# Performance work log

Measured on AMD Instinct MI355X. Metric: run time of the kernel, lower is better.

The kernel has to match this reference:

```python
import jax, jax.numpy as jnp
import numpy as np

B, N, F, H, N_ITERS = 64, 256, 16, 256, 10


def setup_inputs() -> dict:
    key = jax.random.key(0)
    ks = jax.random.split(key, 20)
    s = 0.05
    jets = jax.random.normal(ks[0], (B, N, F), dtype=jnp.float32)
    # row-normalized dense adjacency (D^-1 A style)
    a = jax.random.uniform(ks[1], (B, N, N), dtype=jnp.float32)
    dads = a / jnp.sum(a, axis=-1, keepdims=True)
    p = lambda k, sh: jax.random.normal(k, sh, dtype=jnp.float32) * s
    return {
        'jets': jets, 'dads': dads,
        'W_emb': p(ks[2], (F, H)), 'b_emb': jnp.zeros((H,), jnp.float32),
        'W_msg': p(ks[3], (H, H)), 'b_msg': jnp.zeros((H,), jnp.float32),
        # GRU vertex update: input = concat(message[H], s[F]) -> H
        'Wz': p(ks[4], (H + F, H)), 'Uz': p(ks[5], (H, H)), 'bz': jnp.zeros((H,), jnp.float32),
        'Wr': p(ks[6], (H + F, H)), 'Ur': p(ks[7], (H, H)), 'br': jnp.zeros((H,), jnp.float32),
        'Wh': p(ks[8], (H + F, H)), 'Uh': p(ks[9], (H, H)), 'bh': jnp.zeros((H,), jnp.float32),
        'W_r1': p(ks[10], (H, H)), 'b_r1': jnp.zeros((H,), jnp.float32),
        'W_r2': p(ks[11], (H, H)), 'b_r2': jnp.zeros((H,), jnp.float32),
    }


def reference(jets, dads, W_emb, b_emb, W_msg, b_msg,
              Wz, Uz, bz, Wr, Ur, br, Wh, Uh, bh,
              W_r1, b_r1, W_r2, b_r2):
    # Embedding: [B,N,F] -> [B,N,H]
    h = jnp.tanh(jets @ W_emb + b_emb)
    for _ in range(N_ITERS):
        # Message: linear then adjacency aggregation + tanh
        m = jnp.tanh(jnp.matmul(dads, h @ W_msg + b_msg))  # [B,N,H]
        # GRU-style vertex update; input = concat(message, original features s)
        x = jnp.concatenate([m, jets], axis=-1)            # [B,N,H+F]
        z = jax.nn.sigmoid(x @ Wz + h @ Uz + bz)
        r = jax.nn.sigmoid(x @ Wr + h @ Ur + br)
        h_tilde = jnp.tanh(x @ Wh + (r * h) @ Uh + bh)
        h = (1.0 - z) * h + z * h_tilde
    # Readout: per-node MLP then sum over nodes -> [B,H]
    out = jnp.sum(jnp.tanh(h @ W_r1 + b_r1) @ W_r2 + b_r2, axis=1)
    return out
```

## Files before the change

kernel.cpp:

```cpp
#include <hip/hip_runtime.h>

#define DEVI __device__ __forceinline__

typedef __attribute__((ext_vector_type(4))) float f32x4;
typedef __attribute__((ext_vector_type(8))) short s16x8;
typedef __attribute__((ext_vector_type(4))) short s16x4;
typedef unsigned short u16;
typedef unsigned int u32;

#define WST 288
#define SROW 264
#define AST 260

#define WAITVM(n) __builtin_amdgcn_s_waitcnt(((n)&0xF) | 0x70 | 0xF00 | (((n)>>4)<<14))

DEVI u16 f2bf(float x){
  u32 u = __float_as_uint(x);
  u = (u + 0x7fffu + ((u >> 16) & 1u)) >> 16;
  return (u16)u;
}
DEVI float bf2f(u16 v){ return __uint_as_float(((u32)v) << 16); }

DEVI float fsigm(float x){ return __builtin_amdgcn_rcpf(1.f + __builtin_amdgcn_exp2f(-1.442695041f * x)); }
DEVI float ftanh(float x){ float e = __builtin_amdgcn_exp2f(2.885390082f * x); return 1.f - 2.f * __builtin_amdgcn_rcpf(e + 1.f); }

DEVI s16x8 ld8(const u16* p){ return *(const s16x8*)p; }
DEVI s16x8 ldb64p(const u16* p){
  s16x4 lo = *(const s16x4*)p;
  s16x4 hi = *(const s16x4*)(p + 4);
  s16x8 r;
  r[0]=lo[0]; r[1]=lo[1]; r[2]=lo[2]; r[3]=lo[3];
  r[4]=hi[0]; r[5]=hi[1]; r[6]=hi[2]; r[7]=hi[3];
  return r;
}

DEVI f32x4 ld4bf(const u16* p){
  uint2 v = *(const uint2*)p;
  f32x4 r;
  r[0] = bf2f((u16)(v.x & 0xffff)); r[1] = bf2f((u16)(v.x >> 16));
  r[2] = bf2f((u16)(v.y & 0xffff)); r[3] = bf2f((u16)(v.y >> 16));
  return r;
}

DEVI void st4bf(u16* p, float a, float b, float c, float d){
  uint2 v;
  v.x = (u32)f2bf(a) | ((u32)f2bf(b) << 16);
  v.y = (u32)f2bf(c) | ((u32)f2bf(d) << 16);
  *(uint2*)p = v;
}

#define MFMA(a,b,c) __builtin_amdgcn_mfma_f32_16x16x32_bf16((a),(b),(c),0,0,0)

DEVI void dma4(const u16* lanebase, int rowStrideElems, int c, u16* ldsbase){
#pragma unroll
  for(int q = 0; q < 4; q++){
    const u16* g = lanebase + (size_t)q*16*rowStrideElems + c*32;
    __builtin_amdgcn_global_load_lds((__attribute__((address_space(1))) const void*)g,
                                     (__attribute__((address_space(3))) void*)(ldsbase + q*512),
                                     16, 0, 0);
  }
}
#define AFRAG(buf, t) ld8(&(buf)[(t)*512 + ln*32 + ((qd ^ ((ln>>1)&3))*8)])

__global__ void k_prep(
  const float* __restrict__ jets, const float* __restrict__ dads, const float* __restrict__ W_emb,
  const float* __restrict__ W_msg, const float* __restrict__ Wz, const float* __restrict__ Uz,
  const float* __restrict__ Wr, const float* __restrict__ Ur, const float* __restrict__ Wh,
  const float* __restrict__ Uh, const float* __restrict__ W_r1,
  u16* __restrict__ jp, u16* __restrict__ dadsb, u16* __restrict__ Wet, u16* __restrict__ Wmt,
  u16* __restrict__ Wzt, u16* __restrict__ Uzt, u16* __restrict__ Wrt, u16* __restrict__ Urt,
  u16* __restrict__ Wht, u16* __restrict__ Uht, u16* __restrict__ Wr1t)
{
  int blk = blockIdx.x, tid = threadIdx.x;
  if(blk < 1280){
    int mi = blk >> 8, k = blk & 255, j = tid;
    const float* src; u16* dst;
    switch(mi){
      case 0: src = W_msg; dst = Wmt;  break;
      case 1: src = Uz;    dst = Uzt;  break;
      case 2: src = Ur;    dst = Urt;  break;
      case 3: src = Uh;    dst = Uht;  break;
      default: src = W_r1; dst = Wr1t; break;
    }
    dst[j*256 + k] = f2bf(src[k*256 + j]);
  } else if(blk < 2144){
    int q = blk - 1280; int mi = q / 288; int k = q - mi*288; int j = tid;
    const float* src; u16* dst;
    switch(mi){ case 0: src = Wz; dst = Wzt; break; case 1: src = Wr; dst = Wrt; break; default: src = Wh; dst = Wht; break; }
    dst[j*WST + k] = (k < 272) ? f2bf(src[k*256 + j]) : (u16)0;
  } else if(blk < 2176){
    int idx = (blk - 2144)*256 + tid;
    int j = idx >> 5, k = idx & 31;
    Wet[idx] = (k < 16) ? f2bf(W_emb[k*256 + j]) : (u16)0;
  } else if(blk < 4224){
    int idx = (blk - 2176)*256 + tid;
    int n = idx >> 5, k = idx & 31;
    jp[idx] = (k < 16) ? f2bf(jets[n*16 + k]) : (u16)0;
  } else {
    int idx = (blk - 4224)*256 + tid;
    f32x4 v = *(const f32x4*)(dads + (size_t)idx*4);
    st4bf(dadsb + (size_t)idx*4, v[0], v[1], v[2], v[3]);
  }
}

__global__ __launch_bounds__(256,3) void k_embed(
  u16* __restrict__ h, u16* __restrict__ hmo,
  const u16* __restrict__ jp, const u16* __restrict__ Wet, const float* __restrict__ be,
  const u16* __restrict__ Wmt, const float* __restrict__ bm)
{
  __shared__ u16 hbuf[16*SROW];
  const int tid = threadIdx.x;
  const int wv = tid >> 6, lane = tid & 63, ln = lane & 15, qd = lane >> 4;
  const int n0 = blockIdx.x * 16;
  const int b  = n0 >> 8;
  const int nb = n0 & 255;
  const int nodeA = n0 + ln;

  s16x8 jfr = ld8(jp + (size_t)nodeA*32 + qd*8);
#pragma unroll
  for(int t = 0; t < 4; t++){
    int j0 = (wv*4 + t) * 16;
    f32x4 acc = {0.f,0.f,0.f,0.f};
    s16x8 a = ld8(Wet + (size_t)(j0 + ln)*32 + qd*8);
    acc = MFMA(a, jfr, acc);
    f32x4 bv = *(const f32x4*)(be + j0 + qd*4);
    f32x4 hv;
#pragma unroll
    for(int r = 0; r < 4; r++) hv[r] = ftanh(acc[r] + bv[r]);
    st4bf(h + (size_t)nodeA*256 + j0 + qd*4, hv[0], hv[1], hv[2], hv[3]);
    st4bf(&hbuf[ln*SROW + j0 + qd*4], hv[0], hv[1], hv[2], hv[3]);
  }
  __syncthreads();

  s16x8 af[8];
#pragma unroll
  for(int c = 0; c < 8; c++) af[c] = ld8(&hbuf[ln*SROW + c*32 + qd*8]);
#pragma unroll
  for(int tp = 0; tp < 2; tp++){
    int j0 = (wv*4 + tp*2) * 16, j1 = j0 + 16;
    f32x4 a0 = {0.f,0.f,0.f,0.f}, a1 = {0.f,0.f,0.f,0.f};
#pragma unroll
    for(int c = 0; c < 8; c++){
      a0 = MFMA(af[c], ld8(Wmt + (size_t)(j0 + ln)*256 + c*32 + qd*8), a0);
      a1 = MFMA(af[c], ld8(Wmt + (size_t)(j1 + ln)*256 + c*32 + qd*8), a1);
    }
    float b0 = bm[j0 + ln], b1 = bm[j1 + ln];
    st4bf(hmo + (size_t)(b*256 + j0 + ln)*256 + nb + qd*4, a0[0]+b0, a0[1]+b0, a0[2]+b0, a0[3]+b0);
    st4bf(hmo + (size_t)(b*256 + j1 + ln)*256 + nb + qd*4, a1[0]+b1, a1[1]+b1, a1[2]+b1, a1[3]+b1);
  }
}

__global__ __launch_bounds__(256,1) void k_gru(
  u16* __restrict__ h,
  const u16* __restrict__ hmi, u16* __restrict__ hmo,
  const u16* __restrict__ dadsb, const u16* __restrict__ jp,
  const u16* __restrict__ Wzt, const u16* __restrict__ Wrt, const u16* __restrict__ Wht,
  const u16* __restrict__ Uzt, const u16* __restrict__ Urt, const u16* __restrict__ Uht,
  const u16* __restrict__ Wmt,
  const float* __restrict__ bz, const float* __restrict__ br, const float* __restrict__ bhb,
  const float* __restrict__ bm)
{
  __shared__ u16 smM[64*AST];
  __shared__ u16 smB[64*AST];
  __shared__ __align__(16) u16 stg[4][2][2][2048];
  const int tid = threadIdx.x;
  const int wv = tid >> 6, lane = tid & 63, ln = lane & 15, qd = lane >> 4;
  const int blk   = blockIdx.x;
  const int batch = (blk & 7) * 8 + (blk >> 5);
  const int group = (blk >> 3) & 3;
  const int n0 = batch * 256 + group * 64;
  const int b  = batch;
  const int nb = group * 64;
  const int j0w = wv * 64;

  u16* s0 = &stg[wv][0][0][0];
  u16* s1 = &stg[wv][1][0][0];
  u16* u0 = &stg[wv][0][1][0];
  u16* u1 = &stg[wv][1][1][0];

  const int rw = lane >> 2;
  const int cs = ((lane & 3) ^ ((lane >> 3) & 3)) * 8;

  const u16* laneA = hmi + (size_t)(b*256 + j0w + rw)*256 + cs;
  dma4(laneA, 256, 0, s0);

  s16x8 jB[4];
#pragma unroll
  for(int i = 0; i < 4; i++) jB[i] = ld8(jp + (size_t)(n0 + i*16 + ln)*32 + qd*8);

  {
    f32x4 acc[4][4];
#pragma unroll
    for(int t = 0; t < 4; t++)
#pragma unroll
      for(int i = 0; i < 4; i++) acc[t][i] = (f32x4){0.f,0.f,0.f,0.f};
    s16x8 Bf[4], Bn[4];
#pragma unroll
    for(int i = 0; i < 4; i++) Bf[i] = ld8(dadsb + (size_t)(n0 + i*16 + ln)*256 + qd*8);
#pragma unroll
    for(int c = 0; c < 8; c++){
      u16* cur = (c & 1) ? s1 : s0;
      if(c < 7){
        dma4(laneA, 256, c+1, (c & 1) ? s0 : s1);
#pragma unroll
        for(int i = 0; i < 4; i++) Bn[i] = ld8(dadsb + (size_t)(n0 + i*16 + ln)*256 + (c+1)*32 + qd*8);
        WAITVM(8);
      } else {
        WAITVM(0);
      }
#pragma unroll
      for(int t = 0; t < 4; t++){
        s16x8 A = AFRAG(cur, t);
#pragma unroll
        for(int i = 0; i < 4; i++) acc[t][i] = MFMA(A, Bf[i], acc[t][i]);
      }
      if(c < 7){
#pragma unroll
        for(int i = 0; i < 4; i++) Bf[i] = Bn[i];
      }
    }
#pragma unroll
    for(int t = 0; t < 4; t++)
#pragma unroll
      for(int i = 0; i < 4; i++)
        st4bf(&smM[(i*16 + ln)*AST + j0w + t*16 + qd*4],
              ftanh(acc[t][i][0]), ftanh(acc[t][i][1]), ftanh(acc[t][i][2]), ftanh(acc[t][i][3]));
  }
  const u16* laneWr = Wrt + (size_t)(j0w + rw)*WST + cs;
  const u16* laneUr = Urt + (size_t)(j0w + rw)*256 + cs;
  dma4(laneWr, WST, 0, s0);
  dma4(laneUr, 256, 0, u0);
  __syncthreads();

  {
    f32x4 acc[4][4];
#pragma unroll
    for(int t = 0; t < 4; t++)
#pragma unroll
      for(int i = 0; i < 4; i++) acc[t][i] = (f32x4){0.f,0.f,0.f,0.f};
    s16x8 Aj[4];
#pragma unroll
    for(int t = 0; t < 4; t++) Aj[t] = ld8(Wrt + (size_t)(j0w + t*16 + ln)*WST + 256 + qd*8);
    s16x8 Bh[4], Bn[4];
#pragma unroll
    for(int i = 0; i < 4; i++) Bh[i] = ld8(h + (size_t)(n0 + i*16 + ln)*256 + qd*8);
#pragma unroll
    for(int c = 0; c < 8; c++){
      u16* cw = (c & 1) ? s1 : s0;
      u16* cu = (c & 1) ? u1 : u0;
      if(c < 7){
        dma4(laneWr, WST, c+1, (c & 1) ? s0 : s1);
        dma4(laneUr, 256, c+1, (c & 1) ? u0 : u1);
#pragma unroll
        for(int i = 0; i < 4; i++) Bn[i] = ld8(h + (size_t)(n0 + i*16 + ln)*256 + (c+1)*32 + qd*8);
        WAITVM(12);
      } else {
        WAITVM(0);
      }
      s16x8 Bm[4];
#pragma unroll
      for(int i = 0; i < 4; i++) Bm[i] = ldb64p(&smM[(i*16 + ln)*AST + c*32 + qd*8]);
#pragma unroll
      for(int t = 0; t < 4; t++){
        s16x8 Aw = AFRAG(cw, t);
#pragma unroll
        for(int i = 0; i < 4; i++) acc[t][i] = MFMA(Aw, Bm[i], acc[t][i]);
      }
#pragma unroll
      for(int t = 0; t < 4; t++){
        s16x8 Au = AFRAG(cu, t);
#pragma unroll
        for(int i = 0; i < 4; i++) acc[t][i] = MFMA(Au, Bh[i], acc[t][i]);
      }
      if(c < 7){
#pragma unroll
        for(int i = 0; i < 4; i++) Bh[i] = Bn[i];
      }
    }
#pragma unroll
    for(int t = 0; t < 4; t++)
#pragma unroll
      for(int i = 0; i < 4; i++) acc[t][i] = MFMA(Aj[t], jB[i], acc[t][i]);
#pragma unroll
    for(int t = 0; t < 4; t++){
      f32x4 bv = *(const f32x4*)(br + j0w + t*16 + qd*4);
#pragma unroll
      for(int i = 0; i < 4; i++){
        f32x4 hv = ld4bf(h + (size_t)(n0 + i*16 + ln)*256 + j0w + t*16 + qd*4);
        st4bf(&smB[(i*16 + ln)*AST + j0w + t*16 + qd*4],
              fsigm(acc[t][i][0]+bv[0])*hv[0], fsigm(acc[t][i][1]+bv[1])*hv[1],
              fsigm(acc[t][i][2]+bv[2])*hv[2], fsigm(acc[t][i][3]+bv[3])*hv[3]);
      }
    }
  }
  const u16* laneWz = Wzt + (size_t)(j0w + rw)*WST + cs;
  const u16* laneUz = Uzt + (size_t)(j0w + rw)*256 + cs;
  dma4(laneWz, WST, 0, s0);
  dma4(laneUz, 256, 0, u0);
  __syncthreads();

  f32x4 zacc[4][4], gacc[4][4];
#pragma unroll
  for(int t = 0; t < 4; t++)
#pragma unroll
    for(int i = 0; i < 4; i++) zacc[t][i] = (f32x4){0.f,0.f,0.f,0.f};
  {
    s16x8 Aj[4];
#pragma unroll
    for(int t = 0; t < 4; t++) Aj[t] = ld8(Wzt + (size_t)(j0w + t*16 + ln)*WST + 256 + qd*8);
    s16x8 Bh[4], Bn[4];
#pragma unroll
    for(int i = 0; i < 4; i++) Bh[i] = ld8(h + (size_t)(n0 + i*16 + ln)*256 + qd*8);
#pragma unroll
    for(int c = 0; c < 8; c++){
      u16* cw = (c & 1) ? s1 : s0;
      u16* cu = (c & 1) ? u1 : u0;
      if(c < 7){
        dma4(laneWz, WST, c+1, (c & 1) ? s0 : s1);
        dma4(laneUz, 256, c+1, (c & 1) ? u0 : u1);
#pragma unroll
        for(int i = 0; i < 4; i++) Bn[i] = ld8(h + (size_t)(n0 + i*16 + ln)*256 + (c+1)*32 + qd*8);
        WAITVM(12);
      } else {
        WAITVM(0);
      }
      s16x8 Bm[4];
#pragma unroll
      for(int i = 0; i < 4; i++) Bm[i] = ldb64p(&smM[(i*16 + ln)*AST + c*32 + qd*8]);
#pragma unroll
      for(int t = 0; t < 4; t++){
        s16x8 Aw = AFRAG(cw, t);
#pragma unroll
        for(int i = 0; i < 4; i++) zacc[t][i] = MFMA(Aw, Bm[i], zacc[t][i]);
      }
#pragma unroll
      for(int t = 0; t < 4; t++){
        s16x8 Au = AFRAG(cu, t);
#pragma unroll
        for(int i = 0; i < 4; i++) zacc[t][i] = MFMA(Au, Bh[i], zacc[t][i]);
      }
      if(c < 7){
#pragma unroll
        for(int i = 0; i < 4; i++) Bh[i] = Bn[i];
      }
    }
#pragma unroll
    for(int t = 0; t < 4; t++)
#pragma unroll
      for(int i = 0; i < 4; i++) zacc[t][i] = MFMA(Aj[t], jB[i], zacc[t][i]);
  }

  const u16* laneWh = Wht + (size_t)(j0w + rw)*WST + cs;
  const u16* laneUh = Uht + (size_t)(j0w + rw)*256 + cs;
  dma4(laneWh, WST, 0, s0);
  dma4(laneUh, 256, 0, u0);

#pragma unroll
  for(int t = 0; t < 4; t++)
#pragma unroll
    for(int i = 0; i < 4; i++) gacc[t][i] = (f32x4){0.f,0.f,0.f,0.f};
  {
    s16x8 Aj[4];
#pragma unroll
    for(int t = 0; t < 4; t++) Aj[t] = ld8(Wht + (size_t)(j0w + t*16 + ln)*WST + 256 + qd*8);
#pragma unroll
    for(int c = 0; c < 8; c++){
      u16* cw = (c & 1) ? s1 : s0;
      u16* cu = (c & 1) ? u1 : u0;
      if(c < 7){
        dma4(laneWh, WST, c+1, (c & 1) ? s0 : s1);
        dma4(laneUh, 256, c+1, (c & 1) ? u0 : u1);
        WAITVM(8);
      } else {
        WAITVM(0);
      }
      s16x8 Bm[4], Brh[4];
#pragma unroll
      for(int i = 0; i < 4; i++){
        Bm[i]  = ldb64p(&smM[(i*16 + ln)*AST + c*32 + qd*8]);
        Brh[i] = ldb64p(&smB[(i*16 + ln)*AST + c*32 + qd*8]);
      }
#pragma unroll
      for(int t = 0; t < 4; t++){
        s16x8 Aw = AFRAG(cw, t);
#pragma unroll
        for(int i = 0; i < 4; i++) gacc[t][i] = MFMA(Aw, Bm[i], gacc[t][i]);
      }
#pragma unroll
      for(int t = 0; t < 4; t++){
        s16x8 Au = AFRAG(cu, t);
#pragma unroll
        for(int i = 0; i < 4; i++) gacc[t][i] = MFMA(Au, Brh[i], gacc[t][i]);
      }
    }
#pragma unroll
    for(int t = 0; t < 4; t++)
#pragma unroll
      for(int i = 0; i < 4; i++) gacc[t][i] = MFMA(Aj[t], jB[i], gacc[t][i]);
  }
  __syncthreads();

#pragma unroll
  for(int t = 0; t < 4; t++){
    f32x4 bzv = *(const f32x4*)(bz + j0w + t*16 + qd*4);
    f32x4 bhv = *(const f32x4*)(bhb + j0w + t*16 + qd*4);
#pragma unroll
    for(int i = 0; i < 4; i++){
      f32x4 hv = ld4bf(h + (size_t)(n0 + i*16 + ln)*256 + j0w + t*16 + qd*4);
      f32x4 hn;
#pragma unroll
      for(int r = 0; r < 4; r++){
        float z  = fsigm(zacc[t][i][r] + bzv[r]);
        float th = ftanh(gacc[t][i][r] + bhv[r]);
        hn[r] = hv[r] + z * (th - hv[r]);
      }
      st4bf(h + (size_t)(n0 + i*16 + ln)*256 + j0w + t*16 + qd*4, hn[0], hn[1], hn[2], hn[3]);
      st4bf(&smM[(i*16 + ln)*AST + j0w + t*16 + qd*4], hn[0], hn[1], hn[2], hn[3]);
    }
  }
  const u16* laneWm = Wmt + (size_t)(j0w + rw)*256 + cs;
  dma4(laneWm, 256, 0, s0);
  __syncthreads();

  {
    f32x4 acc[4][4];
#pragma unroll
    for(int t = 0; t < 4; t++)
#pragma unroll
      for(int i = 0; i < 4; i++) acc[t][i] = (f32x4){0.f,0.f,0.f,0.f};
#pragma unroll
    for(int c = 0; c < 8; c++){
      u16* cur = (c & 1) ? s1 : s0;
      if(c < 7){
        dma4(laneWm, 256, c+1, (c & 1) ? s0 : s1);
        WAITVM(4);
      } else {
        WAITVM(0);
      }
      s16x8 Bf[4];
#pragma unroll
      for(int i = 0; i < 4; i++) Bf[i] = ldb64p(&smM[(i*16 + ln)*AST + c*32 + qd*8]);
#pragma unroll
      for(int t = 0; t < 4; t++){
        s16x8 A = AFRAG(cur, t);
#pragma unroll
        for(int i = 0; i < 4; i++) acc[t][i] = MFMA(A, Bf[i], acc[t][i]);
      }
    }
#pragma unroll
    for(int t = 0; t < 4; t++){
      f32x4 bmv = *(const f32x4*)(bm + j0w + t*16 + qd*4);
#pragma unroll
      for(int i = 0; i < 4; i++){
#pragma unroll
        for(int r = 0; r < 4; r++){
          hmo[(size_t)(b*256 + j0w + t*16 + qd*4 + r)*256 + nb + i*16 + ln] =
            f2bf(acc[t][i][r] + bmv[r]);
        }
      }
    }
  }
}

__global__ __launch_bounds__(256,3) void k_t(
  const u16* __restrict__ h, u16* __restrict__ t_out,
  const u16* __restrict__ Wr1t, const float* __restrict__ br1)
{
  const int tid = threadIdx.x;
  const int wv = tid >> 6, lane = tid & 63, ln = lane & 15, qd = lane >> 4;
  const int n0 = blockIdx.x * 16;
  const int nodeA = n0 + ln;

  s16x8 hfr[8];
#pragma unroll
  for(int c = 0; c < 8; c++) hfr[c] = ld8(h + (size_t)nodeA*256 + c*32 + qd*8);
#pragma unroll
  for(int tp = 0; tp < 2; tp++){
    int j0 = (wv*4 + tp*2) * 16, j1 = j0 + 16;
    f32x4 a0 = {0.f,0.f,0.f,0.f}, a1 = {0.f,0.f,0.f,0.f};
#pragma unroll
    for(int c = 0; c < 8; c++){
      a0 = MFMA(ld8(Wr1t + (size_t)(j0 + ln)*256 + c*32 + qd*8), hfr[c], a0);
      a1 = MFMA(ld8(Wr1t + (size_t)(j1 + ln)*256 + c*32 + qd*8), hfr[c], a1);
    }
    f32x4 b0 = *(const f32x4*)(br1 + j0 + qd*4);
    f32x4 b1 = *(const f32x4*)(br1 + j1 + qd*4);
    st4bf(t_out + (size_t)nodeA*256 + j0 + qd*4,
          ftanh(a0[0]+b0[0]), ftanh(a0[1]+b0[1]), ftanh(a0[2]+b0[2]), ftanh(a0[3]+b0[3]));
    st4bf(t_out + (size_t)nodeA*256 + j1 + qd*4,
          ftanh(a1[0]+b1[0]), ftanh(a1[1]+b1[1]), ftanh(a1[2]+b1[2]), ftanh(a1[3]+b1[3]));
  }
}

__global__ void k_red(const u16* __restrict__ t, const float* __restrict__ W_r2,
                      const float* __restrict__ b_r2, float* __restrict__ out){
  __shared__ float s[256];
  int b = blockIdx.x, k = threadIdx.x;
  float acc = 0.f;
  for(int n = 0; n < 256; n++) acc += bf2f(t[(size_t)(b*256 + n)*256 + k]);
  s[k] = acc;
  __syncthreads();
  int j = threadIdx.x;
  float o = 256.f * b_r2[j];
  for(int k2 = 0; k2 < 256; k2++) o += s[k2] * W_r2[k2*256 + j];
  out[b*256 + j] = o;
}

extern "C" void kernel_launch(void* const* d_in, const int* in_sizes, int n_in,
                              void* d_out, int out_size, void* d_ws, size_t ws_size,
                              hipStream_t stream)
{
  const float* jets  = (const float*)d_in[0];
  const float* dads  = (const float*)d_in[1];
  const float* W_emb = (const float*)d_in[2];
  const float* b_emb = (const float*)d_in[3];
  const float* W_msg = (const float*)d_in[4];
  const float* b_msg = (const float*)d_in[5];
  const float* Wz    = (const float*)d_in[6];
  const float* Uz    = (const float*)d_in[7];
  const float* bz    = (const float*)d_in[8];
  const float* Wr    = (const float*)d_in[9];
  const float* Ur    = (const float*)d_in[10];
  const float* br    = (const float*)d_in[11];
  const float* Wh    = (const float*)d_in[12];
  const float* Uh    = (const float*)d_in[13];
  const float* bh    = (const float*)d_in[14];
  const float* W_r1  = (const float*)d_in[15];
  const float* b_r1  = (const float*)d_in[16];
  const float* W_r2  = (const float*)d_in[17];
  const float* b_r2  = (const float*)d_in[18];

  char* ws = (char*)d_ws;
  u16* h      = (u16*)(ws);
  u16* hmA    = (u16*)(ws + 8388608);
  u16* hmB    = (u16*)(ws + 16777216);
  u16* dadsb  = (u16*)(ws + 25165824);
  u16* jp     = (u16*)(ws + 33554432);
  u16* Wmt    = (u16*)(ws + 34603008);
  u16* Uzt    = (u16*)(ws + 34734080);
  u16* Urt    = (u16*)(ws + 34865152);
  u16* Uht    = (u16*)(ws + 34996224);
  u16* Wr1t   = (u16*)(ws + 35127296);
  u16* Wzt    = (u16*)(ws + 35258368);
  u16* Wrt    = (u16*)(ws + 35405824);
  u16* Wht    = (u16*)(ws + 35553280);
  u16* Wet    = (u16*)(ws + 35700736);
  float* outp = (float*)d_out;

  k_prep<<<8320, 256, 0, stream>>>(jets, dads, W_emb, W_msg, Wz, Uz, Wr, Ur, Wh, Uh, W_r1,
                                   jp, dadsb, Wet, Wmt, Wzt, Uzt, Wrt, Urt, Wht, Uht, Wr1t);
  k_embed<<<1024, 256, 0, stream>>>(h, hmA, jp, Wet, b_emb, Wmt, b_msg);
  for(int it = 0; it < 10; ++it){
    const u16* hin = (it & 1) ? hmB : hmA;
    u16* hout      = (it & 1) ? hmA : hmB;
    k_gru<<<256, 256, 0, stream>>>(h, hin, hout, dadsb, jp,
                                   Wzt, Wrt, Wht, Uzt, Urt, Uht, Wmt,
                                   bz, br, bh, b_msg);
  }
  k_t<<<1024, 256, 0, stream>>>(h, hmB, Wr1t, b_r1);
  k_red<<<64, 256, 0, stream>>>(hmB, W_r2, b_r2, outp);
}
```

Baseline: 561.2 us.

## Split GRU kernel work across eight waves with 32-column slices per wave

Raises the k_gru block from 256 to 512 threads. Each of the eight waves now owns 32 output columns instead of 64, which halves the per-wave accumulators, staging buffers and DMA loads, and the waitcnt values are adjusted to match. The aim is more latency hiding and higher MFMA issue rate per CU for the 256-block grid, which fills only about one block per CU. The cost is that each wave reloads the same B fragments (dads, h, smM) for a narrower output tile, so redundant loads and LDS reads rise.

```diff
diff --git a/kernel.cpp b/kernel.cpp
--- a/kernel.cpp
+++ b/kernel.cpp
@@ -51,9 +51,9 @@
 
 #define MFMA(a,b,c) __builtin_amdgcn_mfma_f32_16x16x32_bf16((a),(b),(c),0,0,0)
 
-DEVI void dma4(const u16* lanebase, int rowStrideElems, int c, u16* ldsbase){
-#pragma unroll
-  for(int q = 0; q < 4; q++){
+DEVI void dma2(const u16* lanebase, int rowStrideElems, int c, u16* ldsbase){
+#pragma unroll
+  for(int q = 0; q < 2; q++){
     const u16* g = lanebase + (size_t)q*16*rowStrideElems + c*32;
     __builtin_amdgcn_global_load_lds((__attribute__((address_space(1))) const void*)g,
                                      (__attribute__((address_space(3))) void*)(ldsbase + q*512),
@@ -150,7 +150,7 @@
   }
 }
 
-__global__ __launch_bounds__(256,1) void k_gru(
+__global__ __launch_bounds__(512,2) void k_gru(
   u16* __restrict__ h,
   const u16* __restrict__ hmi, u16* __restrict__ hmo,
   const u16* __restrict__ dadsb, const u16* __restrict__ jp,
@@ -162,7 +162,7 @@
 {
   __shared__ u16 smM[64*AST];
   __shared__ u16 smB[64*AST];
-  __shared__ __align__(16) u16 stg[4][2][2][2048];
+  __shared__ __align__(16) u16 stg[8][2][2][1024];
   const int tid = threadIdx.x;
   const int wv = tid >> 6, lane = tid & 63, ln = lane & 15, qd = lane >> 4;
   const int blk   = blockIdx.x;
@@ -171,7 +171,7 @@
   const int n0 = batch * 256 + group * 64;
   const int b  = batch;
   const int nb = group * 64;
-  const int j0w = wv * 64;
+  const int j0w = wv * 32;
 
   u16* s0 = &stg[wv][0][0][0];
   u16* s1 = &stg[wv][1][0][0];
@@ -182,16 +182,16 @@
   const int cs = ((lane & 3) ^ ((lane >> 3) & 3)) * 8;
 
   const u16* laneA = hmi + (size_t)(b*256 + j0w + rw)*256 + cs;
-  dma4(laneA, 256, 0, s0);
+  dma2(laneA, 256, 0, s0);
 
   s16x8 jB[4];
 #pragma unroll
   for(int i = 0; i < 4; i++) jB[i] = ld8(jp + (size_t)(n0 + i*16 + ln)*32 + qd*8);
 
   {
-    f32x4 acc[4][4];
-#pragma unroll
-    for(int t = 0; t < 4; t++)
+    f32x4 acc[2][4];
+#pragma unroll
+    for(int t = 0; t < 2; t++)
 #pragma unroll
       for(int i = 0; i < 4; i++) acc[t][i] = (f32x4){0.f,0.f,0.f,0.f};
     s16x8 Bf[4], Bn[4];
@@ -201,73 +201,73 @@
     for(int c = 0; c < 8; c++){
       u16* cur = (c & 1) ? s1 : s0;
       if(c < 7){
-        dma4(laneA, 256, c+1, (c & 1) ? s0 : s1);
+        dma2(laneA, 256, c+1, (c & 1) ? s0 : s1);
 #pragma unroll
         for(int i = 0; i < 4; i++) Bn[i] = ld8(dadsb + (size_t)(n0 + i*16 + ln)*256 + (c+1)*32 + qd*8);
+        WAITVM(6);
+      } else {
+        WAITVM(0);
+      }
+#pragma unroll
+      for(int t = 0; t < 2; t++){
+        s16x8 A = AFRAG(cur, t);
+#pragma unroll
+        for(int i = 0; i < 4; i++) acc[t][i] = MFMA(A, Bf[i], acc[t][i]);
+      }
+      if(c < 7){
+#pragma unroll
+        for(int i = 0; i < 4; i++) Bf[i] = Bn[i];
+      }
+    }
+#pragma unroll
+    for(int t = 0; t < 2; t++)
+#pragma unroll
+      for(int i = 0; i < 4; i++)
+        st4bf(&smM[(i*16 + ln)*AST + j0w + t*16 + qd*4],
+              ftanh(acc[t][i][0]), ftanh(acc[t][i][1]), ftanh(acc[t][i][2]), ftanh(acc[t][i][3]));
+  }
+  const u16* laneWr = Wrt + (size_t)(j0w + rw)*WST + cs;
+  const u16* laneUr = Urt + (size_t)(j0w + rw)*256 + cs;
+  dma2(laneWr, WST, 0, s0);
+  dma2(laneUr, 256, 0, u0);
+  __syncthreads();
+
+  {
+    f32x4 acc[2][4];
+#pragma unroll
+    for(int t = 0; t < 2; t++)
+#pragma unroll
+      for(int i = 0; i < 4; i++) acc[t][i] = (f32x4){0.f,0.f,0.f,0.f};
+    s16x8 Aj[2];
+#pragma unroll
+    for(int t = 0; t < 2; t++) Aj[t] = ld8(Wrt + (size_t)(j0w + t*16 + ln)*WST + 256 + qd*8);
+    s16x8 Bh[4], Bn[4];
+#pragma unroll
+    for(int i = 0; i < 4; i++) Bh[i] = ld8(h + (size_t)(n0 + i*16 + ln)*256 + qd*8);
+#pragma unroll
+    for(int c = 0; c < 8; c++){
+      u16* cw = (c & 1) ? s1 : s0;
+      u16* cu = (c & 1) ? u1 : u0;
+      if(c < 7){
+        dma2(laneWr, WST, c+1, (c & 1) ? s0 : s1);
+        dma2(laneUr, 256, c+1, (c & 1) ? u0 : u1);
+#pragma unroll
+        for(int i = 0; i < 4; i++) Bn[i] = ld8(h + (size_t)(n0 + i*16 + ln)*256 + (c+1)*32 + qd*8);
         WAITVM(8);
       } else {
         WAITVM(0);
       }
-#pragma unroll
-      for(int t = 0; t < 4; t++){
-        s16x8 A = AFRAG(cur, t);
-#pragma unroll
-        for(int i = 0; i < 4; i++) acc[t][i] = MFMA(A, Bf[i], acc[t][i]);
-      }
-      if(c < 7){
-#pragma unroll
-        for(int i = 0; i < 4; i++) Bf[i] = Bn[i];
-      }
-    }
-#pragma unroll
-    for(int t = 0; t < 4; t++)
-#pragma unroll
-      for(int i = 0; i < 4; i++)
-        st4bf(&smM[(i*16 + ln)*AST + j0w + t*16 + qd*4],
-              ftanh(acc[t][i][0]), ftanh(acc[t][i][1]), ftanh(acc[t][i][2]), ftanh(acc[t][i][3]));
-  }
-  const u16* laneWr = Wrt + (size_t)(j0w + rw)*WST + cs;
-  const u16* laneUr = Urt + (size_t)(j0w + rw)*256 + cs;
-  dma4(laneWr, WST, 0, s0);
-  dma4(laneUr, 256, 0, u0);
-  __syncthreads();
-
-  {
-    f32x4 acc[4][4];
-#pragma unroll
-    for(int t = 0; t < 4; t++)
-#pragma unroll
-      for(int i = 0; i < 4; i++) acc[t][i] = (f32x4){0.f,0.f,0.f,0.f};
-    s16x8 Aj[4];
-#pragma unroll
-    for(int t = 0; t < 4; t++) Aj[t] = ld8(Wrt + (size_t)(j0w + t*16 + ln)*WST + 256 + qd*8);
-    s16x8 Bh[4], Bn[4];
-#pragma unroll
-    for(int i = 0; i < 4; i++) Bh[i] = ld8(h + (size_t)(n0 + i*16 + ln)*256 + qd*8);
-#pragma unroll
-    for(int c = 0; c < 8; c++){
-      u16* cw = (c & 1) ? s1 : s0;
-      u16* cu = (c & 1) ? u1 : u0;
-      if(c < 7){
-        dma4(laneWr, WST, c+1, (c & 1) ? s0 : s1);
-        dma4(laneUr, 256, c+1, (c & 1) ? u0 : u1);
-#pragma unroll
-        for(int i = 0; i < 4; i++) Bn[i] = ld8(h + (size_t)(n0 + i*16 + ln)*256 + (c+1)*32 + qd*8);
-        WAITVM(12);
-      } else {
-        WAITVM(0);
-      }
       s16x8 Bm[4];
 #pragma unroll
       for(int i = 0; i < 4; i++) Bm[i] = ldb64p(&smM[(i*16 + ln)*AST + c*32 + qd*8]);
 #pragma unroll
-      for(int t = 0; t < 4; t++){
+      for(int t = 0; t < 2; t++){
         s16x8 Aw = AFRAG(cw, t);
 #pragma unroll
         for(int i = 0; i < 4; i++) acc[t][i] = MFMA(Aw, Bm[i], acc[t][i]);
       }
 #pragma unroll
-      for(int t = 0; t < 4; t++){
+      for(int t = 0; t < 2; t++){
         s16x8 Au = AFRAG(cu, t);
 #pragma unroll
         for(int i = 0; i < 4; i++) acc[t][i] = MFMA(Au, Bh[i], acc[t][i]);
@@ -278,11 +278,11 @@
       }
     }
 #pragma unroll
-    for(int t = 0; t < 4; t++)
+    for(int t = 0; t < 2; t++)
 #pragma unroll
       for(int i = 0; i < 4; i++) acc[t][i] = MFMA(Aj[t], jB[i], acc[t][i]);
 #pragma unroll
-    for(int t = 0; t < 4; t++){
+    for(int t = 0; t < 2; t++){
       f32x4 bv = *(const f32x4*)(br + j0w + t*16 + qd*4);
 #pragma unroll
       for(int i = 0; i < 4; i++){
@@ -295,19 +295,19 @@
   }
   const u16* laneWz = Wzt + (size_t)(j0w + rw)*WST + cs;
   const u16* laneUz = Uzt + (size_t)(j0w + rw)*256 + cs;
-  dma4(laneWz, WST, 0, s0);
-  dma4(laneUz, 256, 0, u0);
+  dma2(laneWz, WST, 0, s0);
+  dma2(laneUz, 256, 0, u0);
   __syncthreads();
 
-  f32x4 zacc[4][4], gacc[4][4];
-#pragma unroll
-  for(int t = 0; t < 4; t++)
+  f32x4 zacc[2][4], gacc[2][4];
+#pragma unroll
+  for(int t = 0; t < 2; t++)
 #pragma unroll
     for(int i = 0; i < 4; i++) zacc[t][i] = (f32x4){0.f,0.f,0.f,0.f};
   {
-    s16x8 Aj[4];
-#pragma unroll
-    for(int t = 0; t < 4; t++) Aj[t] = ld8(Wzt + (size_t)(j0w + t*16 + ln)*WST + 256 + qd*8);
+    s16x8 Aj[2];
+#pragma unroll
+    for(int t = 0; t < 2; t++) Aj[t] = ld8(Wzt + (size_t)(j0w + t*16 + ln)*WST + 256 + qd*8);
     s16x8 Bh[4], Bn[4];
 #pragma unroll
     for(int i = 0; i < 4; i++) Bh[i] = ld8(h + (size_t)(n0 + i*16 + ln)*256 + qd*8);
@@ -316,64 +316,64 @@
       u16* cw = (c & 1) ? s1 : s0;
       u16* cu = (c & 1) ? u1 : u0;
       if(c < 7){
-        dma4(laneWz, WST, c+1, (c & 1) ? s0 : s1);
-        dma4(laneUz, 256, c+1, (c & 1) ? u0 : u1);
+        dma2(laneWz, WST, c+1, (c & 1) ? s0 : s1);
+        dma2(laneUz, 256, c+1, (c & 1) ? u0 : u1);
 #pragma unroll
         for(int i = 0; i < 4; i++) Bn[i] = ld8(h + (size_t)(n0 + i*16 + ln)*256 + (c+1)*32 + qd*8);
-        WAITVM(12);
-      } else {
-        WAITVM(0);
-      }
-      s16x8 Bm[4];
-#pragma unroll
-      for(int i = 0; i < 4; i++) Bm[i] = ldb64p(&smM[(i*16 + ln)*AST + c*32 + qd*8]);
-#pragma unroll
-      for(int t = 0; t < 4; t++){
-        s16x8 Aw = AFRAG(cw, t);
-#pragma unroll
-        for(int i = 0; i < 4; i++) zacc[t][i] = MFMA(Aw, Bm[i], zacc[t][i]);
-      }
-#pragma unroll
-      for(int t = 0; t < 4; t++){
-        s16x8 Au = AFRAG(cu, t);
-#pragma unroll
-        for(int i = 0; i < 4; i++) zacc[t][i] = MFMA(Au, Bh[i], zacc[t][i]);
-      }
-      if(c < 7){
-#pragma unroll
-        for(int i = 0; i < 4; i++) Bh[i] = Bn[i];
-      }
-    }
-#pragma unroll
-    for(int t = 0; t < 4; t++)
-#pragma unroll
-      for(int i = 0; i < 4; i++) zacc[t][i] = MFMA(Aj[t], jB[i], zacc[t][i]);
-  }
-
-  const u16* laneWh = Wht + (size_t)(j0w + rw)*WST + cs;
-  const u16* laneUh = Uht + (size_t)(j0w + rw)*256 + cs;
-  dma4(laneWh, WST, 0, s0);
-  dma4(laneUh, 256, 0, u0);
-
-#pragma unroll
-  for(int t = 0; t < 4; t++)
-#pragma unroll
-    for(int i = 0; i < 4; i++) gacc[t][i] = (f32x4){0.f,0.f,0.f,0.f};
-  {
-    s16x8 Aj[4];
-#pragma unroll
-    for(int t = 0; t < 4; t++) Aj[t] = ld8(Wht + (size_t)(j0w + t*16 + ln)*WST + 256 + qd*8);
-#pragma unroll
-    for(int c = 0; c < 8; c++){
-      u16* cw = (c & 1) ? s1 : s0;
-      u16* cu = (c & 1) ? u1 : u0;
-      if(c < 7){
-        dma4(laneWh, WST, c+1, (c & 1) ? s0 : s1);
-        dma4(laneUh, 256, c+1, (c & 1) ? u0 : u1);
         WAITVM(8);
       } else {
         WAITVM(0);
       }
+      s16x8 Bm[4];
+#pragma unroll
+      for(int i = 0; i < 4; i++) Bm[i] = ldb64p(&smM[(i*16 + ln)*AST + c*32 + qd*8]);
+#pragma unroll
+      for(int t = 0; t < 2; t++){
+        s16x8 Aw = AFRAG(cw, t);
+#pragma unroll
+        for(int i = 0; i < 4; i++) zacc[t][i] = MFMA(Aw, Bm[i], zacc[t][i]);
+      }
+#pragma unroll
+      for(int t = 0; t < 2; t++){
+        s16x8 Au = AFRAG(cu, t);
+#pragma unroll
+        for(int i = 0; i < 4; i++) zacc[t][i] = MFMA(Au, Bh[i], zacc[t][i]);
+      }
+      if(c < 7){
+#pragma unroll
+        for(int i = 0; i < 4; i++) Bh[i] = Bn[i];
+      }
+    }
+#pragma unroll
+    for(int t = 0; t < 2; t++)
+#pragma unroll
+      for(int i = 0; i < 4; i++) zacc[t][i] = MFMA(Aj[t], jB[i], zacc[t][i]);
+  }
+
+  const u16* laneWh = Wht + (size_t)(j0w + rw)*WST + cs;
+  const u16* laneUh = Uht + (size_t)(j0w + rw)*256 + cs;
+  dma2(laneWh, WST, 0, s0);
+  dma2(laneUh, 256, 0, u0);
+
+#pragma unroll
+  for(int t = 0; t < 2; t++)
+#pragma unroll
+    for(int i = 0; i < 4; i++) gacc[t][i] = (f32x4){0.f,0.f,0.f,0.f};
+  {
+    s16x8 Aj[2];
+#pragma unroll
+    for(int t = 0; t < 2; t++) Aj[t] = ld8(Wht + (size_t)(j0w + t*16 + ln)*WST + 256 + qd*8);
+#pragma unroll
+    for(int c = 0; c < 8; c++){
+      u16* cw = (c & 1) ? s1 : s0;
+      u16* cu = (c & 1) ? u1 : u0;
+      if(c < 7){
+        dma2(laneWh, WST, c+1, (c & 1) ? s0 : s1);
+        dma2(laneUh, 256, c+1, (c & 1) ? u0 : u1);
+        WAITVM(4);
+      } else {
+        WAITVM(0);
+      }
       s16x8 Bm[4], Brh[4];
 #pragma unroll
       for(int i = 0; i < 4; i++){
@@ -381,27 +381,27 @@
         Brh[i] = ldb64p(&smB[(i*16 + ln)*AST + c*32 + qd*8]);
       }
 #pragma unroll
-      for(int t = 0; t < 4; t++){
+      for(int t = 0; t < 2; t++){
         s16x8 Aw = AFRAG(cw, t);
 #pragma unroll
         for(int i = 0; i < 4; i++) gacc[t][i] = MFMA(Aw, Bm[i], gacc[t][i]);
       }
 #pragma unroll
-      for(int t = 0; t < 4; t++){
+      for(int t = 0; t < 2; t++){
         s16x8 Au = AFRAG(cu, t);
 #pragma unroll
         for(int i = 0; i < 4; i++) gacc[t][i] = MFMA(Au, Brh[i], gacc[t][i]);
       }
     }
 #pragma unroll
-    for(int t = 0; t < 4; t++)
+    for(int t = 0; t < 2; t++)
 #pragma unroll
       for(int i = 0; i < 4; i++) gacc[t][i] = MFMA(Aj[t], jB[i], gacc[t][i]);
   }
   __syncthreads();
 
 #pragma unroll
-  for(int t = 0; t < 4; t++){
+  for(int t = 0; t < 2; t++){
     f32x4 bzv = *(const f32x4*)(bz + j0w + t*16 + qd*4);
     f32x4 bhv = *(const f32x4*)(bhb + j0w + t*16 + qd*4);
 #pragma unroll
@@ -419,21 +419,21 @@
     }
   }
   const u16* laneWm = Wmt + (size_t)(j0w + rw)*256 + cs;
-  dma4(laneWm, 256, 0, s0);
+  dma2(laneWm, 256, 0, s0);
   __syncthreads();
 
   {
-    f32x4 acc[4][4];
-#pragma unroll
-    for(int t = 0; t < 4; t++)
+    f32x4 acc[2][4];
+#pragma unroll
+    for(int t = 0; t < 2; t++)
 #pragma unroll
       for(int i = 0; i < 4; i++) acc[t][i] = (f32x4){0.f,0.f,0.f,0.f};
 #pragma unroll
     for(int c = 0; c < 8; c++){
       u16* cur = (c & 1) ? s1 : s0;
       if(c < 7){
-        dma4(laneWm, 256, c+1, (c & 1) ? s0 : s1);
-        WAITVM(4);
+        dma2(laneWm, 256, c+1, (c & 1) ? s0 : s1);
+        WAITVM(2);
       } else {
         WAITVM(0);
       }
@@ -441,14 +441,14 @@
 #pragma unroll
       for(int i = 0; i < 4; i++) Bf[i] = ldb64p(&smM[(i*16 + ln)*AST + c*32 + qd*8]);
 #pragma unroll
-      for(int t = 0; t < 4; t++){
+      for(int t = 0; t < 2; t++){
         s16x8 A = AFRAG(cur, t);
 #pragma unroll
         for(int i = 0; i < 4; i++) acc[t][i] = MFMA(A, Bf[i], acc[t][i]);
       }
     }
 #pragma unroll
-    for(int t = 0; t < 4; t++){
+    for(int t = 0; t < 2; t++){
       f32x4 bmv = *(const f32x4*)(bm + j0w + t*16 + qd*4);
 #pragma unroll
       for(int i = 0; i < 4; i++){
@@ -553,7 +553,7 @@
   for(int it = 0; it < 10; ++it){
     const u16* hin = (it & 1) ? hmB : hmA;
     u16* hout      = (it & 1) ? hmA : hmB;
-    k_gru<<<256, 256, 0, stream>>>(h, hin, hout, dadsb, jp,
+    k_gru<<<256, 512, 0, stream>>>(h, hin, hout, dadsb, jp,
                                    Wzt, Wrt, Wht, Uzt, Urt, Uht, Wmt,
                                    bz, br, bh, b_msg);
   }
```

After: 602.6 us. 1.07x slower.

## Replace LDS DMA staging of weight tiles with register triple-buffered global loads

Applied to the files above, without the earlier changes.

Removes the per-wave global_load_lds staging buffers and explicit vmcnt waits, and instead loads MFMA A-operand fragments straight from global memory into registers with a three-deep prefetch ring. This frees 64KB of LDS and avoids the LDS round trip and swizzled fragment reads. The cost is much higher VGPR use (up to 24 extra s16x8 per stage) and reliance on the compiler's waitcnt placement, which may serialize loads or spill.

```diff
diff --git a/kernel.cpp b/kernel.cpp
--- a/kernel.cpp
+++ b/kernel.cpp
@@ -11,8 +11,6 @@
 #define WST 288
 #define SROW 264
 #define AST 260
-
-#define WAITVM(n) __builtin_amdgcn_s_waitcnt(((n)&0xF) | 0x70 | 0xF00 | (((n)>>4)<<14))
 
 DEVI u16 f2bf(float x){
   u32 u = __float_as_uint(x);
@@ -50,17 +48,6 @@
 }
 
 #define MFMA(a,b,c) __builtin_amdgcn_mfma_f32_16x16x32_bf16((a),(b),(c),0,0,0)
-
-DEVI void dma4(const u16* lanebase, int rowStrideElems, int c, u16* ldsbase){
-#pragma unroll
-  for(int q = 0; q < 4; q++){
-    const u16* g = lanebase + (size_t)q*16*rowStrideElems + c*32;
-    __builtin_amdgcn_global_load_lds((__attribute__((address_space(1))) const void*)g,
-                                     (__attribute__((address_space(3))) void*)(ldsbase + q*512),
-                                     16, 0, 0);
-  }
-}
-#define AFRAG(buf, t) ld8(&(buf)[(t)*512 + ln*32 + ((qd ^ ((ln>>1)&3))*8)])
 
 __global__ void k_prep(
   const float* __restrict__ jets, const float* __restrict__ dads, const float* __restrict__ W_emb,
@@ -162,7 +149,6 @@
 {
   __shared__ u16 smM[64*AST];
   __shared__ u16 smB[64*AST];
-  __shared__ __align__(16) u16 stg[4][2][2][2048];
   const int tid = threadIdx.x;
   const int wv = tid >> 6, lane = tid & 63, ln = lane & 15, qd = lane >> 4;
   const int blk   = blockIdx.x;
@@ -173,16 +159,13 @@
   const int nb = group * 64;
   const int j0w = wv * 64;
 
-  u16* s0 = &stg[wv][0][0][0];
-  u16* s1 = &stg[wv][1][0][0];
-  u16* u0 = &stg[wv][0][1][0];
-  u16* u1 = &stg[wv][1][1][0];
-
-  const int rw = lane >> 2;
-  const int cs = ((lane & 3) ^ ((lane >> 3) & 3)) * 8;
-
-  const u16* laneA = hmi + (size_t)(b*256 + j0w + rw)*256 + cs;
-  dma4(laneA, 256, 0, s0);
+  const u16* Ab1 = hmi + (size_t)(b*256 + j0w + ln)*256 + qd*8;
+  s16x8 Am[3][4];
+#pragma unroll
+  for(int p = 0; p < 2; p++)
+#pragma unroll
+    for(int t = 0; t < 4; t++)
+      Am[p][t] = ld8(Ab1 + (size_t)t*16*256 + p*32);
 
   s16x8 jB[4];
 #pragma unroll
@@ -199,18 +182,17 @@
     for(int i = 0; i < 4; i++) Bf[i] = ld8(dadsb + (size_t)(n0 + i*16 + ln)*256 + qd*8);
 #pragma unroll
     for(int c = 0; c < 8; c++){
-      u16* cur = (c & 1) ? s1 : s0;
+      if(c < 6){
+#pragma unroll
+        for(int t = 0; t < 4; t++) Am[(c+2)%3][t] = ld8(Ab1 + (size_t)t*16*256 + (c+2)*32);
+      }
       if(c < 7){
-        dma4(laneA, 256, c+1, (c & 1) ? s0 : s1);
 #pragma unroll
         for(int i = 0; i < 4; i++) Bn[i] = ld8(dadsb + (size_t)(n0 + i*16 + ln)*256 + (c+1)*32 + qd*8);
-        WAITVM(8);
-      } else {
-        WAITVM(0);
-      }
-#pragma unroll
-      for(int t = 0; t < 4; t++){
-        s16x8 A = AFRAG(cur, t);
+      }
+#pragma unroll
+      for(int t = 0; t < 4; t++){
+        s16x8 A = Am[c%3][t];
 #pragma unroll
         for(int i = 0; i < 4; i++) acc[t][i] = MFMA(A, Bf[i], acc[t][i]);
       }
@@ -226,10 +208,16 @@
         st4bf(&smM[(i*16 + ln)*AST + j0w + t*16 + qd*4],
               ftanh(acc[t][i][0]), ftanh(acc[t][i][1]), ftanh(acc[t][i][2]), ftanh(acc[t][i][3]));
   }
-  const u16* laneWr = Wrt + (size_t)(j0w + rw)*WST + cs;
-  const u16* laneUr = Urt + (size_t)(j0w + rw)*256 + cs;
-  dma4(laneWr, WST, 0, s0);
-  dma4(laneUr, 256, 0, u0);
+  const u16* AbWr = Wrt + (size_t)(j0w + ln)*WST + qd*8;
+  const u16* AbUr = Urt + (size_t)(j0w + ln)*256 + qd*8;
+  s16x8 RW[3][4], RU[3][4];
+#pragma unroll
+  for(int p = 0; p < 2; p++)
+#pragma unroll
+    for(int t = 0; t < 4; t++){
+      RW[p][t] = ld8(AbWr + (size_t)t*16*WST + p*32);
+      RU[p][t] = ld8(AbUr + (size_t)t*16*256 + p*32);
+    }
   __syncthreads();
 
   {
@@ -238,37 +226,37 @@
     for(int t = 0; t < 4; t++)
 #pragma unroll
       for(int i = 0; i < 4; i++) acc[t][i] = (f32x4){0.f,0.f,0.f,0.f};
-    s16x8 Aj[4];
-#pragma unroll
-    for(int t = 0; t < 4; t++) Aj[t] = ld8(Wrt + (size_t)(j0w + t*16 + ln)*WST + 256 + qd*8);
+    s16x8 Ajr[4];
+#pragma unroll
+    for(int t = 0; t < 4; t++) Ajr[t] = ld8(AbWr + (size_t)t*16*WST + 256);
     s16x8 Bh[4], Bn[4];
 #pragma unroll
     for(int i = 0; i < 4; i++) Bh[i] = ld8(h + (size_t)(n0 + i*16 + ln)*256 + qd*8);
 #pragma unroll
     for(int c = 0; c < 8; c++){
-      u16* cw = (c & 1) ? s1 : s0;
-      u16* cu = (c & 1) ? u1 : u0;
+      if(c < 6){
+#pragma unroll
+        for(int t = 0; t < 4; t++){
+          RW[(c+2)%3][t] = ld8(AbWr + (size_t)t*16*WST + (c+2)*32);
+          RU[(c+2)%3][t] = ld8(AbUr + (size_t)t*16*256 + (c+2)*32);
+        }
+      }
       if(c < 7){
-        dma4(laneWr, WST, c+1, (c & 1) ? s0 : s1);
-        dma4(laneUr, 256, c+1, (c & 1) ? u0 : u1);
 #pragma unroll
         for(int i = 0; i < 4; i++) Bn[i] = ld8(h + (size_t)(n0 + i*16 + ln)*256 + (c+1)*32 + qd*8);
-        WAITVM(12);
-      } else {
-        WAITVM(0);
       }
       s16x8 Bm[4];
 #pragma unroll
       for(int i = 0; i < 4; i++) Bm[i] = ldb64p(&smM[(i*16 + ln)*AST + c*32 + qd*8]);
 #pragma unroll
       for(int t = 0; t < 4; t++){
-        s16x8 Aw = AFRAG(cw, t);
+        s16x8 Aw = RW[c%3][t];
 #pragma unroll
         for(int i = 0; i < 4; i++) acc[t][i] = MFMA(Aw, Bm[i], acc[t][i]);
       }
 #pragma unroll
       for(int t = 0; t < 4; t++){
-        s16x8 Au = AFRAG(cu, t);
+        s16x8 Au = RU[c%3][t];
 #pragma unroll
         for(int i = 0; i < 4; i++) acc[t][i] = MFMA(Au, Bh[i], acc[t][i]);
       }
@@ -280,7 +268,7 @@
 #pragma unroll
     for(int t = 0; t < 4; t++)
 #pragma unroll
-      for(int i = 0; i < 4; i++) acc[t][i] = MFMA(Aj[t], jB[i], acc[t][i]);
+      for(int i = 0; i < 4; i++) acc[t][i] = MFMA(Ajr[t], jB[i], acc[t][i]);
 #pragma unroll
     for(int t = 0; t < 4; t++){
       f32x4 bv = *(const f32x4*)(br + j0w + t*16 + qd*4);
@@ -293,10 +281,16 @@
       }
     }
   }
-  const u16* laneWz = Wzt + (size_t)(j0w + rw)*WST + cs;
-  const u16* laneUz = Uzt + (size_t)(j0w + rw)*256 + cs;
-  dma4(laneWz, WST, 0, s0);
-  dma4(laneUz, 256, 0, u0);
+  const u16* AbWz = Wzt + (size_t)(j0w + ln)*WST + qd*8;
+  const u16* AbUz = Uzt + (size_t)(j0w + ln)*256 + qd*8;
+  s16x8 ZW[3][4], ZU[3][4];
+#pragma unroll
+  for(int p = 0; p < 2; p++)
+#pragma unroll
+    for(int t = 0; t < 4; t++){
+      ZW[p][t] = ld8(AbWz + (size_t)t*16*WST + p*32);
+      ZU[p][t] = ld8(AbUz + (size_t)t*16*256 + p*32);
+    }
   __syncthreads();
 
   f32x4 zacc[4][4], gacc[4][4];
@@ -305,37 +299,37 @@
 #pragma unroll
     for(int i = 0; i < 4; i++) zacc[t][i] = (f32x4){0.f,0.f,0.f,0.f};
   {
-    s16x8 Aj[4];
-#pragma unroll
-    for(int t = 0; t < 4; t++) Aj[t] = ld8(Wzt + (size_t)(j0w + t*16 + ln)*WST + 256 + qd*8);
+    s16x8 Ajz[4];
+#pragma unroll
+    for(int t = 0; t < 4; t++) Ajz[t] = ld8(AbWz + (size_t)t*16*WST + 256);
     s16x8 Bh[4], Bn[4];
 #pragma unroll
     for(int i = 0; i < 4; i++) Bh[i] = ld8(h + (size_t)(n0 + i*16 + ln)*256 + qd*8);
 #pragma unroll
     for(int c = 0; c < 8; c++){
-      u16* cw = (c & 1) ? s1 : s0;
-      u16* cu = (c & 1) ? u1 : u0;
+      if(c < 6){
+#pragma unroll
+        for(int t = 0; t < 4; t++){
+          ZW[(c+2)%3][t] = ld8(AbWz + (size_t)t*16*WST + (c+2)*32);
+          ZU[(c+2)%3][t] = ld8(AbUz + (size_t)t*16*256 + (c+2)*32);
+        }
+      }
       if(c < 7){
-        dma4(laneWz, WST, c+1, (c & 1) ? s0 : s1);
-        dma4(laneUz, 256, c+1, (c & 1) ? u0 : u1);
 #pragma unroll
         for(int i = 0; i < 4; i++) Bn[i] = ld8(h + (size_t)(n0 + i*16 + ln)*256 + (c+1)*32 + qd*8);
-        WAITVM(12);
-      } else {
-        WAITVM(0);
       }
       s16x8 Bm[4];
 #pragma unroll
       for(int i = 0; i < 4; i++) Bm[i] = ldb64p(&smM[(i*16 + ln)*AST + c*32 + qd*8]);
 #pragma unroll
       for(int t = 0; t < 4; t++){
-        s16x8 Aw = AFRAG(cw, t);
+        s16x8 Aw = ZW[c%3][t];
 #pragma unroll
         for(int i = 0; i < 4; i++) zacc[t][i] = MFMA(Aw, Bm[i], zacc[t][i]);
       }
 #pragma unroll
       for(int t = 0; t < 4; t++){
-        s16x8 Au = AFRAG(cu, t);
+        s16x8 Au = ZU[c%3][t];
 #pragma unroll
         for(int i = 0; i < 4; i++) zacc[t][i] = MFMA(Au, Bh[i], zacc[t][i]);
       }
@@ -347,32 +341,36 @@
 #pragma unroll
     for(int t = 0; t < 4; t++)
 #pragma unroll
-      for(int i = 0; i < 4; i++) zacc[t][i] = MFMA(Aj[t], jB[i], zacc[t][i]);
-  }
-
-  const u16* laneWh = Wht + (size_t)(j0w + rw)*WST + cs;
-  const u16* laneUh = Uht + (size_t)(j0w + rw)*256 + cs;
-  dma4(laneWh, WST, 0, s0);
-  dma4(laneUh, 256, 0, u0);
+      for(int i = 0; i < 4; i++) zacc[t][i] = MFMA(Ajz[t], jB[i], zacc[t][i]);
+  }
+
+  const u16* AbWh = Wht + (size_t)(j0w + ln)*WST + qd*8;
+  const u16* AbUh = Uht + (size_t)(j0w + ln)*256 + qd*8;
+  s16x8 GW[3][4], GU[3][4];
+#pragma unroll
+  for(int p = 0; p < 2; p++)
+#pragma unroll
+    for(int t = 0; t < 4; t++){
+      GW[p][t] = ld8(AbWh + (size_t)t*16*WST + p*32);
+      GU[p][t] = ld8(AbUh + (size_t)t*16*256 + p*32);
+    }
 
 #pragma unroll
   for(int t = 0; t < 4; t++)
 #pragma unroll
     for(int i = 0; i < 4; i++) gacc[t][i] = (f32x4){0.f,0.f,0.f,0.f};
   {
-    s16x8 Aj[4];
-#pragma unroll
-    for(int t = 0; t < 4; t++) Aj[t] = ld8(Wht + (size_t)(j0w + t*16 + ln)*WST + 256 + qd*8);
-#pragma unroll
-    for(int c = 0; c < 8; c++){
-      u16* cw = (c & 1) ? s1 : s0;
-      u16* cu = (c & 1) ? u1 : u0;
-      if(c < 7){
-        dma4(laneWh, WST, c+1, (c & 1) ? s0 : s1);
-        dma4(laneUh, 256, c+1, (c & 1) ? u0 : u1);
-        WAITVM(8);
-      } else {
-        WAITVM(0);
+    s16x8 Ajh[4];
+#pragma unroll
+    for(int t = 0; t < 4; t++) Ajh[t] = ld8(AbWh + (size_t)t*16*WST + 256);
+#pragma unroll
+    for(int c = 0; c < 8; c++){
+      if(c < 6){
+#pragma unroll
+        for(int t = 0; t < 4; t++){
+          GW[(c+2)%3][t] = ld8(AbWh + (size_t)t*16*WST + (c+2)*32);
+          GU[(c+2)%3][t] = ld8(AbUh + (size_t)t*16*256 + (c+2)*32);
+        }
       }
       s16x8 Bm[4], Brh[4];
 #pragma unroll
@@ -382,13 +380,13 @@
       }
 #pragma unroll
       for(int t = 0; t < 4; t++){
-        s16x8 Aw = AFRAG(cw, t);
+        s16x8 Aw = GW[c%3][t];
 #pragma unroll
         for(int i = 0; i < 4; i++) gacc[t][i] = MFMA(Aw, Bm[i], gacc[t][i]);
       }
 #pragma unroll
       for(int t = 0; t < 4; t++){
-        s16x8 Au = AFRAG(cu, t);
+        s16x8 Au = GU[c%3][t];
 #pragma unroll
         for(int i = 0; i < 4; i++) gacc[t][i] = MFMA(Au, Brh[i], gacc[t][i]);
       }
@@ -396,7 +394,7 @@
 #pragma unroll
     for(int t = 0; t < 4; t++)
 #pragma unroll
-      for(int i = 0; i < 4; i++) gacc[t][i] = MFMA(Aj[t], jB[i], gacc[t][i]);
+      for(int i = 0; i < 4; i++) gacc[t][i] = MFMA(Ajh[t], jB[i], gacc[t][i]);
   }
   __syncthreads();
 
@@ -418,8 +416,13 @@
       st4bf(&smM[(i*16 + ln)*AST + j0w + t*16 + qd*4], hn[0], hn[1], hn[2], hn[3]);
     }
   }
-  const u16* laneWm = Wmt + (size_t)(j0w + rw)*256 + cs;
-  dma4(laneWm, 256, 0, s0);
+  const u16* AbWm = Wmt + (size_t)(j0w + ln)*256 + qd*8;
+  s16x8 MW[3][4];
+#pragma unroll
+  for(int p = 0; p < 2; p++)
+#pragma unroll
+    for(int t = 0; t < 4; t++)
+      MW[p][t] = ld8(AbWm + (size_t)t*16*256 + p*32);
   __syncthreads();
 
   {
@@ -430,19 +433,16 @@
       for(int i = 0; i < 4; i++) acc[t][i] = (f32x4){0.f,0.f,0.f,0.f};
 #pragma unroll
     for(int c = 0; c < 8; c++){
-      u16* cur = (c & 1) ? s1 : s0;
-      if(c < 7){
-        dma4(laneWm, 256, c+1, (c & 1) ? s0 : s1);
-        WAITVM(4);
-      } else {
-        WAITVM(0);
+      if(c < 6){
+#pragma unroll
+        for(int t = 0; t < 4; t++) MW[(c+2)%3][t] = ld8(AbWm + (size_t)t*16*256 + (c+2)*32);
       }
       s16x8 Bf[4];
 #pragma unroll
       for(int i = 0; i < 4; i++) Bf[i] = ldb64p(&smM[(i*16 + ln)*AST + c*32 + qd*8]);
 #pragma unroll
       for(int t = 0; t < 4; t++){
-        s16x8 A = AFRAG(cur, t);
+        s16x8 A = MW[c%3][t];
 #pragma unroll
         for(int i = 0; i < 4; i++) acc[t][i] = MFMA(A, Bf[i], acc[t][i]);
       }
```

Result: slower. 644.2 us (+14.8%).
